# Performance work log

Hardware: AMD Instinct MI355X
Metric: run time of the kernel (lower is better)

The kernel has to match this reference:

```python
import jax, jax.numpy as jnp
import numpy as np

B, L, D, H = 4, 1024, 1024, 16
DK = D // H


def setup_inputs() -> dict:
    key = jax.random.key(0)
    ks = jax.random.split(key, 5)
    s = 1.0 / np.sqrt(D)  # roughly nn.Linear init scale
    return {
        "x": jax.random.normal(ks[0], (B, L, D), dtype=jnp.float32),
        "Wq": jax.random.normal(ks[1], (D, D), dtype=jnp.float32) * s,
        "bq": jnp.zeros((D,), dtype=jnp.float32),
        "Wk": jax.random.normal(ks[2], (D, D), dtype=jnp.float32) * s,
        "bk": jnp.zeros((D,), dtype=jnp.float32),
        "Wv": jax.random.normal(ks[3], (D, D), dtype=jnp.float32) * s,
        "bv": jnp.zeros((D,), dtype=jnp.float32),
        "Wo": jax.random.normal(ks[4], (D, D), dtype=jnp.float32) * s,
        "bo": jnp.zeros((D,), dtype=jnp.float32),
    }


def reference(x, Wq, bq, Wk, bk, Wv, bv, Wo, bo):
    b, l, d = x.shape
    # torch Linear: y = x @ W.T + b
    q = (x @ Wq.T + bq).reshape(b, l, H, DK).transpose(0, 2, 1, 3)  # [B,H,L,DK]
    k = (x @ Wk.T + bk).reshape(b, l, H, DK).transpose(0, 2, 1, 3)
    v = (x @ Wv.T + bv).reshape(b, l, H, DK).transpose(0, 2, 1, 3)
    scores = jnp.einsum("bhqd,bhkd->bhqk", q, k) / jnp.sqrt(jnp.float32(DK))
    attn = jax.nn.softmax(scores, axis=-1)  # dropout p=0 -> identity
    head_out = jnp.einsum("bhqk,bhkd->bhqd", attn, v)  # [B,H,L,DK]
    merged = head_out.transpose(0, 2, 1, 3).reshape(b, l, d)  # [B,L,D]
    out = merged @ Wo.T + bo
    # DeCov loss over head outputs
    U = merged.reshape(b * l, d)
    U = U - U.mean(axis=0, keepdims=True)
    C = (U.T @ U) / jnp.float32(b * l)
    decov = 0.5 * (jnp.sum(C * C) - jnp.sum(jnp.diag(C) ** 2))
    return (out, decov)
```

## Files before the change

### kernel.cpp

```cpp
#include <hip/hip_runtime.h>
#include <cstdint>
#include <cstddef>

typedef short v4s __attribute__((ext_vector_type(4)));
typedef short v8s __attribute__((ext_vector_type(8)));
typedef float v4f __attribute__((ext_vector_type(4)));

__device__ __forceinline__ short f2bf(float f) {
    union { float f; unsigned u; } x; x.f = f;
    unsigned r = (x.u + 0x7FFFu + ((x.u >> 16) & 1u)) >> 16;
    return (short)(unsigned short)r;
}
__device__ __forceinline__ float bf2f(short h) {
    union { unsigned u; float f; } x; x.u = ((unsigned)(unsigned short)h) << 16;
    return x.f;
}

__device__ __forceinline__ void gld16(const void* g, void* l) {
    __builtin_amdgcn_global_load_lds((const __attribute__((address_space(1))) void*)g,
                                     (__attribute__((address_space(3))) void*)l, 16, 0, 0);
}

__global__ __launch_bounds__(256) void cvt_bf16(
    const float* __restrict__ x, const float* __restrict__ wq, const float* __restrict__ wk,
    const float* __restrict__ wv, const float* __restrict__ wo,
    short* __restrict__ xb, short* __restrict__ wqb, short* __restrict__ wkb,
    short* __restrict__ wvb, short* __restrict__ wob)
{
    int bid = blockIdx.x;
    const float* src; short* dst; size_t base;
    if (bid < 4096)      { src = x;  dst = xb;  base = (size_t)bid * 1024; }
    else if (bid < 5120) { src = wq; dst = wqb; base = (size_t)(bid - 4096) * 1024; }
    else if (bid < 6144) { src = wk; dst = wkb; base = (size_t)(bid - 5120) * 1024; }
    else if (bid < 7168) { src = wv; dst = wvb; base = (size_t)(bid - 6144) * 1024; }
    else                 { src = wo; dst = wob; base = (size_t)(bid - 7168) * 1024; }
    size_t idx = base + (size_t)threadIdx.x * 4;
    v4f v = *(const v4f*)(src + idx);
    v4s o;
    o[0] = f2bf(v[0]); o[1] = f2bf(v[1]); o[2] = f2bf(v[2]); o[3] = f2bf(v[3]);
    *(v4s*)(dst + idx) = o;
}

__global__ __launch_bounds__(256) void gemm_qkv(
    const short* __restrict__ xb,
    const short* __restrict__ wq, const short* __restrict__ wk, const short* __restrict__ wv,
    const float* __restrict__ bq, const float* __restrict__ bk, const float* __restrict__ bv,
    short* __restrict__ qo, short* __restrict__ ko, short* __restrict__ vto)
{
    __shared__ __align__(16) short At[128 * 32];
    __shared__ __align__(16) short Bt[128 * 32];
    const int K = 1024;
    const int mode = blockIdx.z;
    const short* W = (mode == 0) ? wq : (mode == 1) ? wk : wv;
    const float* bias = (mode == 0) ? bq : (mode == 1) ? bk : bv;
    const int m0 = blockIdx.y * 128, n0 = blockIdx.x * 128;
    const int tid = threadIdx.x, wave = tid >> 6, lane = tid & 63;
    const int quad = lane >> 4, ll = lane & 15;
    const int wr = wave >> 1, wc = wave & 1;
    const v4f zero4 = {0.f, 0.f, 0.f, 0.f};
    v4f acc[4][4];
    for (int i = 0; i < 4; ++i) for (int j = 0; j < 4; ++j) acc[i][j] = zero4;

    for (int k0 = 0; k0 < K; k0 += 32) {
        __syncthreads();
#pragma unroll
        for (int c = 0; c < 2; ++c) {
            int chb = (wave * 2 + c) * 64;
            int ch = chb + lane;
            int row = ch >> 2, col8 = (ch & 3) * 8;
            gld16(xb + (size_t)(m0 + row) * K + k0 + col8, &At[chb * 8]);
            gld16(W  + (size_t)(n0 + row) * K + k0 + col8, &Bt[chb * 8]);
        }
        __syncthreads();
        v8s af[4], bfr[4];
#pragma unroll
        for (int i = 0; i < 4; ++i) af[i]  = *(const v8s*)&At[(wr * 64 + i * 16 + ll) * 32 + quad * 8];
#pragma unroll
        for (int j = 0; j < 4; ++j) bfr[j] = *(const v8s*)&Bt[(wc * 64 + j * 16 + ll) * 32 + quad * 8];
#pragma unroll
        for (int i = 0; i < 4; ++i)
#pragma unroll
            for (int j = 0; j < 4; ++j)
                acc[i][j] = __builtin_amdgcn_mfma_f32_16x16x32_bf16(af[i], bfr[j], acc[i][j], 0, 0, 0);
    }

    const float scale = (mode == 0) ? 0.125f : 1.0f;
#pragma unroll
    for (int j = 0; j < 4; ++j) {
        int n = n0 + wc * 64 + j * 16 + ll;
        float bb = bias[n];
        int hh = n >> 6, dk = n & 63;
#pragma unroll
        for (int i = 0; i < 4; ++i) {
            int mbase = m0 + wr * 64 + i * 16 + quad * 4;
#pragma unroll
            for (int r = 0; r < 4; ++r) {
                int m = mbase + r;
                int b = m >> 10, li = m & 1023;
                short h = f2bf((acc[i][j][r] + bb) * scale);
                if (mode == 0)
                    qo[(((size_t)(b * 16 + hh) * 1024 + li) << 6) + dk] = h;
                else if (mode == 1)
                    ko[(((size_t)(b * 16 + hh) * 1024 + li) << 6) + dk] = h;
                else
                    vto[(((size_t)(b * 16 + hh) * 64 + dk) << 10) + li] = h;
            }
        }
    }
}

__global__ __launch_bounds__(256) void gemm_out(
    const short* __restrict__ A, const short* __restrict__ W,
    const float* __restrict__ bias, float* __restrict__ out)
{
    __shared__ __align__(16) short At[128 * 32];
    __shared__ __align__(16) short Bt[128 * 32];
    const int K = 1024;
    const int m0 = blockIdx.y * 128, n0 = blockIdx.x * 128;
    const int tid = threadIdx.x, wave = tid >> 6, lane = tid & 63;
    const int quad = lane >> 4, ll = lane & 15;
    const int wr = wave >> 1, wc = wave & 1;
    const v4f zero4 = {0.f, 0.f, 0.f, 0.f};
    v4f acc[4][4];
    for (int i = 0; i < 4; ++i) for (int j = 0; j < 4; ++j) acc[i][j] = zero4;

    for (int k0 = 0; k0 < K; k0 += 32) {
        __syncthreads();
#pragma unroll
        for (int c = 0; c < 2; ++c) {
            int chb = (wave * 2 + c) * 64;
            int ch = chb + lane;
            int row = ch >> 2, col8 = (ch & 3) * 8;
            gld16(A + (size_t)(m0 + row) * K + k0 + col8, &At[chb * 8]);
            gld16(W + (size_t)(n0 + row) * K + k0 + col8, &Bt[chb * 8]);
        }
        __syncthreads();
        v8s af[4], bfr[4];
#pragma unroll
        for (int i = 0; i < 4; ++i) af[i]  = *(const v8s*)&At[(wr * 64 + i * 16 + ll) * 32 + quad * 8];
#pragma unroll
        for (int j = 0; j < 4; ++j) bfr[j] = *(const v8s*)&Bt[(wc * 64 + j * 16 + ll) * 32 + quad * 8];
#pragma unroll
        for (int i = 0; i < 4; ++i)
#pragma unroll
            for (int j = 0; j < 4; ++j)
                acc[i][j] = __builtin_amdgcn_mfma_f32_16x16x32_bf16(af[i], bfr[j], acc[i][j], 0, 0, 0);
    }

#pragma unroll
    for (int j = 0; j < 4; ++j) {
        int n = n0 + wc * 64 + j * 16 + ll;
        float bb = bias[n];
#pragma unroll
        for (int i = 0; i < 4; ++i) {
            int mbase = m0 + wr * 64 + i * 16 + quad * 4;
#pragma unroll
            for (int r = 0; r < 4; ++r) {
                int m = mbase + r;
                out[(size_t)m * 1024 + n] = acc[i][j][r] + bb;
            }
        }
    }
}

__global__ __launch_bounds__(256) void attn_flash(
    const short* __restrict__ qb, const short* __restrict__ kb, const short* __restrict__ vtb,
    float* __restrict__ merged, short* __restrict__ mergedh)
{
    __shared__ __align__(16) short Kt[64 * 64];
    __shared__ __align__(16) short Vt[64 * 64];
    __shared__ __align__(16) short Pt[4 * 16 * 68];
    const int bh = blockIdx.y, qt = blockIdx.x;
    const int tid = threadIdx.x, wave = tid >> 6, lane = tid & 63;
    const int quad = lane >> 4, ll = lane & 15;
    const short* qp = qb  + (size_t)bh * 1024 * 64;
    const short* kp = kb  + (size_t)bh * 1024 * 64;
    const short* vp = vtb + (size_t)bh * 64 * 1024;

    const int qrow = qt * 64 + wave * 16 + ll;
    v8s qa0 = *(const v8s*)(qp + (size_t)qrow * 64 + quad * 8);
    v8s qa1 = *(const v8s*)(qp + (size_t)qrow * 64 + 32 + quad * 8);

    const v4f zero4 = {0.f, 0.f, 0.f, 0.f};
    v4f oacc[4];
    for (int nt = 0; nt < 4; ++nt) oacc[nt] = zero4;
    float lsum[4] = {0.f, 0.f, 0.f, 0.f};
    short* pw = &Pt[wave * 16 * 68];

    for (int jt = 0; jt < 16; ++jt) {
        __syncthreads();
#pragma unroll
        for (int c = 0; c < 2; ++c) {
            int chb = (wave * 2 + c) * 64;
            int ch = chb + lane;
            int row = ch >> 3;
            int gi = ((ch & 7) ^ (row & 7)) * 8;
            gld16(kp + (size_t)(jt * 64 + row) * 64 + gi, &Kt[chb * 8]);
            gld16(vp + (size_t)row * 1024 + jt * 64 + gi, &Vt[chb * 8]);
        }
        __syncthreads();

        v4f sacc[4];
#pragma unroll
        for (int nt = 0; nt < 4; ++nt) {
            int n = nt * 16 + ll;
            int g0 = (quad ^ (n & 7)) * 8;
            int g1 = ((4 + quad) ^ (n & 7)) * 8;
            v8s b0 = *(const v8s*)&Kt[n * 64 + g0];
            v8s b1 = *(const v8s*)&Kt[n * 64 + g1];
            v4f s = zero4;
            s = __builtin_amdgcn_mfma_f32_16x16x32_bf16(qa0, b0, s, 0, 0, 0);
            s = __builtin_amdgcn_mfma_f32_16x16x32_bf16(qa1, b1, s, 0, 0, 0);
            sacc[nt] = s;
        }
#pragma unroll
        for (int nt = 0; nt < 4; ++nt) {
#pragma unroll
            for (int r = 0; r < 4; ++r) {
                float e = __expf(sacc[nt][r]);
                lsum[r] += e;
                pw[(quad * 4 + r) * 68 + nt * 16 + ll] = f2bf(e);
            }
        }
        __syncthreads();
        v4s p00 = *(const v4s*)&pw[ll * 68 + quad * 8];
        v4s p01 = *(const v4s*)&pw[ll * 68 + quad * 8 + 4];
        v4s p10 = *(const v4s*)&pw[ll * 68 + 32 + quad * 8];
        v4s p11 = *(const v4s*)&pw[ll * 68 + 32 + quad * 8 + 4];
        v8s pa0 = __builtin_shufflevector(p00, p01, 0, 1, 2, 3, 4, 5, 6, 7);
        v8s pa1 = __builtin_shufflevector(p10, p11, 0, 1, 2, 3, 4, 5, 6, 7);
#pragma unroll
        for (int nt = 0; nt < 4; ++nt) {
            int n = nt * 16 + ll;
            int g0 = (quad ^ (n & 7)) * 8;
            int g1 = ((4 + quad) ^ (n & 7)) * 8;
            v8s v0 = *(const v8s*)&Vt[n * 64 + g0];
            v8s v1 = *(const v8s*)&Vt[n * 64 + g1];
            oacc[nt] = __builtin_amdgcn_mfma_f32_16x16x32_bf16(pa0, v0, oacc[nt], 0, 0, 0);
            oacc[nt] = __builtin_amdgcn_mfma_f32_16x16x32_bf16(pa1, v1, oacc[nt], 0, 0, 0);
        }
    }

    float linv[4];
#pragma unroll
    for (int r = 0; r < 4; ++r) {
        float s = lsum[r];
        s += __shfl_xor(s, 1); s += __shfl_xor(s, 2);
        s += __shfl_xor(s, 4); s += __shfl_xor(s, 8);
        linv[r] = 1.0f / s;
    }
    const int b = bh >> 4, h = bh & 15;
#pragma unroll
    for (int r = 0; r < 4; ++r) {
        int li = qt * 64 + wave * 16 + quad * 4 + r;
        size_t rowoff = ((size_t)(b * 1024 + li)) * 1024 + h * 64;
#pragma unroll
        for (int nt = 0; nt < 4; ++nt) {
            int d = nt * 16 + ll;
            float v = oacc[nt][r] * linv[r];
            merged[rowoff + d] = v;
            mergedh[rowoff + d] = f2bf(v);
        }
    }
}

__global__ __launch_bounds__(256) void col_part(const float* __restrict__ merged, float* __restrict__ part) {
    const int bi = blockIdx.x, t = threadIdx.x;
    const float* base = merged + (size_t)bi * 128 * 1024 + (size_t)t * 4;
    float s0 = 0.f, s1 = 0.f, s2 = 0.f, s3 = 0.f;
    for (int r = 0; r < 128; ++r) {
        v4f v = *(const v4f*)(base + (size_t)r * 1024);
        s0 += v[0]; s1 += v[1]; s2 += v[2]; s3 += v[3];
    }
    v4f o = {s0, s1, s2, s3};
    *(v4f*)(part + (size_t)bi * 1024 + (size_t)t * 4) = o;
}

__global__ __launch_bounds__(256) void col_mean(const float* __restrict__ part, float* __restrict__ mean) {
    int c = blockIdx.x * 256 + threadIdx.x;
    float s = 0.f;
    for (int i = 0; i < 32; ++i) s += part[i * 1024 + c];
    mean[c] = s * (1.0f / 4096.0f);
}

__global__ __launch_bounds__(256) void center_tr(
    const float* __restrict__ merged, const float* __restrict__ cmean,
    short* __restrict__ uth, short* __restrict__ utl)
{
    __shared__ short Hh[64][72];
    __shared__ short Hl[64][72];
    const int d0 = blockIdx.x * 64, m0 = blockIdx.y * 64;
    const int t = threadIdx.x;
    const int r0 = t >> 4, c4 = (t & 15) * 4;
    float mu[4];
#pragma unroll
    for (int e = 0; e < 4; ++e) mu[e] = cmean[d0 + c4 + e];
    for (int rr = 0; rr < 64; rr += 16) {
        int m = m0 + rr + r0;
        v4f v = *(const v4f*)(merged + (size_t)m * 1024 + d0 + c4);
#pragma unroll
        for (int e = 0; e < 4; ++e) {
            float u = v[e] - mu[e];
            short h = f2bf(u);
            Hh[c4 + e][rr + r0] = h;
            Hl[c4 + e][rr + r0] = f2bf(u - bf2f(h));
        }
    }
    __syncthreads();
    const int d = t >> 2, mg = (t & 3) * 16;
    v8s a0, a1, b0, b1;
#pragma unroll
    for (int e = 0; e < 8; ++e) {
        a0[e] = Hh[d][mg + e]; a1[e] = Hh[d][mg + 8 + e];
        b0[e] = Hl[d][mg + e]; b1[e] = Hl[d][mg + 8 + e];
    }
    size_t off = (size_t)(d0 + d) * 4096 + m0 + mg;
    *(v8s*)(uth + off) = a0; *(v8s*)(uth + off + 8) = a1;
    *(v8s*)(utl + off) = b0; *(v8s*)(utl + off + 8) = b1;
}

__global__ __launch_bounds__(256) void gemm_decov(
    const short* __restrict__ uth, const short* __restrict__ utl, float* __restrict__ dpart)
{
    const int I = blockIdx.y, J = blockIdx.x;
    const int tid = threadIdx.x;
    if (J < I) { if (tid == 0) dpart[I * 16 + J] = 0.f; return; }
    __shared__ __align__(16) short Ah[64 * 32], Al[64 * 32], Bh[64 * 32], Bl[64 * 32];
    __shared__ float wsums[4];
    const int wave = tid >> 6, lane = tid & 63;
    const int quad = lane >> 4, ll = lane & 15;
    const int wr = wave >> 1, wc = wave & 1;
    const v4f zero4 = {0.f, 0.f, 0.f, 0.f};
    v4f acc[2][2];
    for (int i = 0; i < 2; ++i) for (int j = 0; j < 2; ++j) acc[i][j] = zero4;

    for (int k0 = 0; k0 < 4096; k0 += 32) {
        __syncthreads();
        {
            int ch = wave * 64 + lane;
            int row = ch >> 2, col8 = (ch & 3) * 8;
            gld16(uth + (size_t)(I * 64 + row) * 4096 + k0 + col8, &Ah[wave * 512]);
            gld16(utl + (size_t)(I * 64 + row) * 4096 + k0 + col8, &Al[wave * 512]);
            gld16(uth + (size_t)(J * 64 + row) * 4096 + k0 + col8, &Bh[wave * 512]);
            gld16(utl + (size_t)(J * 64 + row) * 4096 + k0 + col8, &Bl[wave * 512]);
        }
        __syncthreads();
        v8s ah[2], al[2], bh[2], bl[2];
#pragma unroll
        for (int i = 0; i < 2; ++i) {
            int ro = (wr * 32 + i * 16 + ll) * 32 + quad * 8;
            ah[i] = *(const v8s*)&Ah[ro];
            al[i] = *(const v8s*)&Al[ro];
        }
#pragma unroll
        for (int j = 0; j < 2; ++j) {
            int ro = (wc * 32 + j * 16 + ll) * 32 + quad * 8;
            bh[j] = *(const v8s*)&Bh[ro];
            bl[j] = *(const v8s*)&Bl[ro];
        }
#pragma unroll
        for (int i = 0; i < 2; ++i)
#pragma unroll
            for (int j = 0; j < 2; ++j) {
                acc[i][j] = __builtin_amdgcn_mfma_f32_16x16x32_bf16(ah[i], bh[j], acc[i][j], 0, 0, 0);
                acc[i][j] = __builtin_amdgcn_mfma_f32_16x16x32_bf16(ah[i], bl[j], acc[i][j], 0, 0, 0);
                acc[i][j] = __builtin_amdgcn_mfma_f32_16x16x32_bf16(al[i], bh[j], acc[i][j], 0, 0, 0);
            }
    }

    float s = 0.f;
#pragma unroll
    for (int i = 0; i < 2; ++i)
#pragma unroll
        for (int j = 0; j < 2; ++j)
#pragma unroll
            for (int r = 0; r < 4; ++r) {
                int gi = I * 64 + wr * 32 + i * 16 + quad * 4 + r;
                int gj = J * 64 + wc * 32 + j * 16 + ll;
                float cv = acc[i][j][r];
                if (gi != gj) s += cv * cv;
            }
    s += __shfl_xor(s, 1); s += __shfl_xor(s, 2); s += __shfl_xor(s, 4);
    s += __shfl_xor(s, 8); s += __shfl_xor(s, 16); s += __shfl_xor(s, 32);
    if (lane == 0) wsums[wave] = s;
    __syncthreads();
    if (tid == 0) {
        float tot = wsums[0] + wsums[1] + wsums[2] + wsums[3];
        dpart[I * 16 + J] = (I < J) ? 2.f * tot : tot;
    }
}

__global__ __launch_bounds__(256) void decov_final(const float* __restrict__ dpart, float* __restrict__ out) {
    const int t = threadIdx.x;
    __shared__ float wsums[4];
    float s = dpart[t];
    s += __shfl_xor(s, 1); s += __shfl_xor(s, 2); s += __shfl_xor(s, 4);
    s += __shfl_xor(s, 8); s += __shfl_xor(s, 16); s += __shfl_xor(s, 32);
    if ((t & 63) == 0) wsums[t >> 6] = s;
    __syncthreads();
    if (t == 0) {
        float tot = wsums[0] + wsums[1] + wsums[2] + wsums[3];
        out[4194304] = 0.5f * tot / (4096.0f * 4096.0f);
    }
}

extern "C" void kernel_launch(void* const* d_in, const int* in_sizes, int n_in,
                              void* d_out, int out_size, void* d_ws, size_t ws_size,
                              hipStream_t stream) {
    const float* x  = (const float*)d_in[0];
    const float* Wq = (const float*)d_in[1];
    const float* bq = (const float*)d_in[2];
    const float* Wk = (const float*)d_in[3];
    const float* bk = (const float*)d_in[4];
    const float* Wv = (const float*)d_in[5];
    const float* bv = (const float*)d_in[6];
    const float* Wo = (const float*)d_in[7];
    const float* bo = (const float*)d_in[8];
    float* out = (float*)d_out;
    char* ws = (char*)d_ws;
    const size_t MB = 1ull << 20;
    short* xb      = (short*)(ws);
    short* wqb     = (short*)(ws + 8  * MB);
    short* wkb     = (short*)(ws + 10 * MB);
    short* wvb     = (short*)(ws + 12 * MB);
    short* wob     = (short*)(ws + 14 * MB);
    short* qb      = (short*)(ws + 16 * MB);
    short* kb      = (short*)(ws + 24 * MB);
    short* vtb     = (short*)(ws + 32 * MB);
    float* merged  = (float*)(ws + 40 * MB);
    short* mergedh = (short*)(ws + 56 * MB);
    float* colpart = (float*)(ws + 64 * MB);
    float* colmean = (float*)(ws + 64 * MB + 256 * 1024);
    short* uth     = (short*)(ws + 65 * MB);
    short* utl     = (short*)(ws + 73 * MB);
    float* dpart   = (float*)(ws + 81 * MB);

    hipLaunchKernelGGL(cvt_bf16, dim3(8192), dim3(256), 0, stream,
                       x, Wq, Wk, Wv, Wo, xb, wqb, wkb, wvb, wob);
    hipLaunchKernelGGL(gemm_qkv, dim3(8, 32, 3), dim3(256), 0, stream,
                       xb, wqb, wkb, wvb, bq, bk, bv, qb, kb, vtb);
    hipLaunchKernelGGL(attn_flash, dim3(16, 64), dim3(256), 0, stream,
                       qb, kb, vtb, merged, mergedh);
    hipLaunchKernelGGL(gemm_out, dim3(8, 32), dim3(256), 0, stream,
                       mergedh, wob, bo, out);
    hipLaunchKernelGGL(col_part, dim3(32), dim3(256), 0, stream, merged, colpart);
    hipLaunchKernelGGL(col_mean, dim3(4), dim3(256), 0, stream, colpart, colmean);
    hipLaunchKernelGGL(center_tr, dim3(16, 64), dim3(256), 0, stream,
                       merged, colmean, uth, utl);
    hipLaunchKernelGGL(gemm_decov, dim3(16, 16), dim3(256), 0, stream, uth, utl, dpart);
    hipLaunchKernelGGL(decov_final, dim3(1), dim3(256), 0, stream, dpart, out);
}
```

Baseline: 273.3 us.

## Split-K the DeCov covariance GEMM over upper-triangle tiles and widen column-mean pass

The covariance GEMM now launches only the 136 upper-triangle tile pairs (no idle lower-triangle blocks) and splits the 4096-long K dimension into 8 chunks, giving 1088 blocks instead of 256 mostly short-lived ones. Partial 64x64 tiles are written to workspace and summed, squared and masked in a new reduce kernel. The column-sum pass also uses 128 blocks of 32 rows instead of 32 blocks of 128 rows. This targets low occupancy in the long serial-K GEMM, at the cost of about 17 MB of extra partial-tile traffic and one more launch. The partials reuse workspace offset 0, which earlier buffers also occupy.

Result: faster. 252.3 us (-7.7%).

```diff
diff --git a/kernel.cpp b/kernel.cpp
--- a/kernel.cpp
+++ b/kernel.cpp
@@ -266,9 +266,9 @@
 
 __global__ __launch_bounds__(256) void col_part(const float* __restrict__ merged, float* __restrict__ part) {
     const int bi = blockIdx.x, t = threadIdx.x;
-    const float* base = merged + (size_t)bi * 128 * 1024 + (size_t)t * 4;
+    const float* base = merged + (size_t)bi * 32 * 1024 + (size_t)t * 4;
     float s0 = 0.f, s1 = 0.f, s2 = 0.f, s3 = 0.f;
-    for (int r = 0; r < 128; ++r) {
+    for (int r = 0; r < 32; ++r) {
         v4f v = *(const v4f*)(base + (size_t)r * 1024);
         s0 += v[0]; s1 += v[1]; s2 += v[2]; s3 += v[3];
     }
@@ -279,7 +279,7 @@
 __global__ __launch_bounds__(256) void col_mean(const float* __restrict__ part, float* __restrict__ mean) {
     int c = blockIdx.x * 256 + threadIdx.x;
     float s = 0.f;
-    for (int i = 0; i < 32; ++i) s += part[i * 1024 + c];
+    for (int i = 0; i < 128; ++i) s += part[i * 1024 + c];
     mean[c] = s * (1.0f / 4096.0f);
 }
 
@@ -320,13 +320,14 @@
 }
 
 __global__ __launch_bounds__(256) void gemm_decov(
-    const short* __restrict__ uth, const short* __restrict__ utl, float* __restrict__ dpart)
-{
-    const int I = blockIdx.y, J = blockIdx.x;
+    const short* __restrict__ uth, const short* __restrict__ utl, float* __restrict__ cpart)
+{
+    int p = blockIdx.x, I = 0, rem = p;
+    while (rem >= 16 - I) { rem -= 16 - I; ++I; }
+    const int J = I + rem;
+    const int kbase = blockIdx.y * 512;
+    __shared__ __align__(16) short Ah[64 * 32], Al[64 * 32], Bh[64 * 32], Bl[64 * 32];
     const int tid = threadIdx.x;
-    if (J < I) { if (tid == 0) dpart[I * 16 + J] = 0.f; return; }
-    __shared__ __align__(16) short Ah[64 * 32], Al[64 * 32], Bh[64 * 32], Bl[64 * 32];
-    __shared__ float wsums[4];
     const int wave = tid >> 6, lane = tid & 63;
     const int quad = lane >> 4, ll = lane & 15;
     const int wr = wave >> 1, wc = wave & 1;
@@ -334,7 +335,8 @@
     v4f acc[2][2];
     for (int i = 0; i < 2; ++i) for (int j = 0; j < 2; ++j) acc[i][j] = zero4;
 
-    for (int k0 = 0; k0 < 4096; k0 += 32) {
+    for (int kk = 0; kk < 512; kk += 32) {
+        int k0 = kbase + kk;
         __syncthreads();
         {
             int ch = wave * 64 + lane;
@@ -368,32 +370,45 @@
             }
     }
 
+    float* dst = cpart + ((size_t)blockIdx.y * 136 + p) * 4096;
+#pragma unroll
+    for (int i = 0; i < 2; ++i)
+#pragma unroll
+        for (int j = 0; j < 2; ++j)
+#pragma unroll
+            for (int r = 0; r < 4; ++r) {
+                int gi2 = wr * 32 + i * 16 + quad * 4 + r;
+                int gj2 = wc * 32 + j * 16 + ll;
+                dst[gi2 * 64 + gj2] = acc[i][j][r];
+            }
+}
+
+__global__ __launch_bounds__(256) void decov_reduce(const float* __restrict__ cpart, float* __restrict__ dsum) {
+    int p = blockIdx.x, I = 0, rem = p;
+    while (rem >= 16 - I) { rem -= 16 - I; ++I; }
+    const int J = I + rem;
+    const int t = threadIdx.x;
+    __shared__ float wsums[4];
     float s = 0.f;
-#pragma unroll
-    for (int i = 0; i < 2; ++i)
-#pragma unroll
-        for (int j = 0; j < 2; ++j)
-#pragma unroll
-            for (int r = 0; r < 4; ++r) {
-                int gi = I * 64 + wr * 32 + i * 16 + quad * 4 + r;
-                int gj = J * 64 + wc * 32 + j * 16 + ll;
-                float cv = acc[i][j][r];
-                if (gi != gj) s += cv * cv;
-            }
+    for (int e = t; e < 4096; e += 256) {
+        float c = 0.f;
+#pragma unroll
+        for (int kc = 0; kc < 8; ++kc) c += cpart[((size_t)kc * 136 + p) * 4096 + e];
+        int gi = I * 64 + (e >> 6), gj = J * 64 + (e & 63);
+        if (gi != gj) s += c * c;
+    }
+    if (I < J) s *= 2.f;
     s += __shfl_xor(s, 1); s += __shfl_xor(s, 2); s += __shfl_xor(s, 4);
     s += __shfl_xor(s, 8); s += __shfl_xor(s, 16); s += __shfl_xor(s, 32);
-    if (lane == 0) wsums[wave] = s;
+    if ((t & 63) == 0) wsums[t >> 6] = s;
     __syncthreads();
-    if (tid == 0) {
-        float tot = wsums[0] + wsums[1] + wsums[2] + wsums[3];
-        dpart[I * 16 + J] = (I < J) ? 2.f * tot : tot;
-    }
-}
-
-__global__ __launch_bounds__(256) void decov_final(const float* __restrict__ dpart, float* __restrict__ out) {
+    if (t == 0) dsum[p] = wsums[0] + wsums[1] + wsums[2] + wsums[3];
+}
+
+__global__ __launch_bounds__(256) void decov_final(const float* __restrict__ dsum, float* __restrict__ out) {
     const int t = threadIdx.x;
     __shared__ float wsums[4];
-    float s = dpart[t];
+    float s = (t < 136) ? dsum[t] : 0.f;
     s += __shfl_xor(s, 1); s += __shfl_xor(s, 2); s += __shfl_xor(s, 4);
     s += __shfl_xor(s, 8); s += __shfl_xor(s, 16); s += __shfl_xor(s, 32);
     if ((t & 63) == 0) wsums[t >> 6] = s;
@@ -430,10 +445,11 @@
     float* merged  = (float*)(ws + 40 * MB);
     short* mergedh = (short*)(ws + 56 * MB);
     float* colpart = (float*)(ws + 64 * MB);
-    float* colmean = (float*)(ws + 64 * MB + 256 * 1024);
+    float* colmean = (float*)(ws + 64 * MB + 512 * 1024);
     short* uth     = (short*)(ws + 65 * MB);
     short* utl     = (short*)(ws + 73 * MB);
-    float* dpart   = (float*)(ws + 81 * MB);
+    float* dsum    = (float*)(ws + 81 * MB);
+    float* cpart   = (float*)(ws);
 
     hipLaunchKernelGGL(cvt_bf16, dim3(8192), dim3(256), 0, stream,
                        x, Wq, Wk, Wv, Wo, xb, wqb, wkb, wvb, wob);
@@ -443,10 +459,11 @@
                        qb, kb, vtb, merged, mergedh);
     hipLaunchKernelGGL(gemm_out, dim3(8, 32), dim3(256), 0, stream,
                        mergedh, wob, bo, out);
-    hipLaunchKernelGGL(col_part, dim3(32), dim3(256), 0, stream, merged, colpart);
+    hipLaunchKernelGGL(col_part, dim3(128), dim3(256), 0, stream, merged, colpart);
     hipLaunchKernelGGL(col_mean, dim3(4), dim3(256), 0, stream, colpart, colmean);
     hipLaunchKernelGGL(center_tr, dim3(16, 64), dim3(256), 0, stream,
                        merged, colmean, uth, utl);
-    hipLaunchKernelGGL(gemm_decov, dim3(16, 16), dim3(256), 0, stream, uth, utl, dpart);
-    hipLaunchKernelGGL(decov_final, dim3(1), dim3(256), 0, stream, dpart, out);
-}
+    hipLaunchKernelGGL(gemm_decov, dim3(136, 8), dim3(256), 0, stream, uth, utl, cpart);
+    hipLaunchKernelGGL(decov_reduce, dim3(136), dim3(256), 0, stream, cpart, dsum);
+    hipLaunchKernelGGL(decov_final, dim3(1), dim3(256), 0, stream, dsum, out);
+}
```
